# Optimization experiments

Measured on AMD Instinct MI355X. Metric: run time of the kernel, lower is better.

Reference implementation:

```python
import jax, jax.numpy as jnp
import numpy as np

ROPE_BASE = 10000.0

def apply_rope(x):
    # x: [B, S, H, Dh]  (rotate-half / NeoX convention)
    B, S, H, Dh = x.shape
    inv_freq = 1.0 / (ROPE_BASE ** (jnp.arange(0, Dh, 2, dtype=jnp.float32) / Dh))  # [Dh/2]
    ang = jnp.arange(S, dtype=jnp.float32)[:, None] * inv_freq[None, :]             # [S, Dh/2]
    cos = jnp.cos(ang)[None, :, None, :].astype(x.dtype)  # [1,S,1,Dh/2]
    sin = jnp.sin(ang)[None, :, None, :].astype(x.dtype)
    x1, x2 = jnp.split(x, 2, axis=-1)
    return jnp.concatenate([x1 * cos - x2 * sin, x1 * sin + x2 * cos], axis=-1)

def setup_inputs() -> dict:
    key = jax.random.key(0)
    k1, k2, k3 = jax.random.split(key, 3)
    B, S, D = 2, 2048, 1024
    x = jax.random.normal(k1, (B, S, D), dtype=jnp.float32)
    attn_mask = jnp.ones((B, S), dtype=bool)
    qkv_w = jax.random.normal(k2, (D, 3 * D), dtype=jnp.float32) * (1.0 / np.sqrt(D))
    out_w = jax.random.normal(k3, (D, D), dtype=jnp.float32) * (1.0 / np.sqrt(D))
    return {"x": x, "qkv_w": qkv_w, "out_w": out_w, "attn_mask": attn_mask, "is_causal": 1}

def reference(x, qkv_w, out_w, attn_mask, is_causal):
    B, S, D = x.shape
    H = 16
    Dh = D // H
    qkv = x @ qkv_w                                  # [B,S,3D]
    q, k, v = jnp.split(qkv, 3, axis=-1)
    q = apply_rope(q.reshape(B, S, H, Dh))           # [B,S,H,Dh]
    k = apply_rope(k.reshape(B, S, H, Dh))
    v = v.reshape(B, S, H, Dh)
    scale = 1.0 / np.sqrt(Dh)
    att = jnp.einsum('bqhd,bkhd->bhqk', q, k) * scale  # [B,H,S,S]
    if is_causal:
        mask = jnp.tril(jnp.ones((S, S), dtype=bool))[None, None]
    else:
        mask = attn_mask[:, None, None, :]             # [B,1,1,S]
    att = jnp.where(mask, att, jnp.finfo(att.dtype).min)
    p = jax.nn.softmax(att, axis=-1)
    y = jnp.einsum('bhqk,bkhd->bqhd', p, v).reshape(B, S, D)
    return y @ out_w
```

## Files before the change

### kernel.cpp

```cpp
#include <hip/hip_runtime.h>
#include <hip/hip_bf16.h>

#define BB 2
#define SS 2048
#define DD 1024
#define HH 16
#define N3 3072

typedef __attribute__((ext_vector_type(8))) short bf16x8;
typedef __attribute__((ext_vector_type(4))) float f32x4;

__device__ __forceinline__ float b2f(unsigned short u) {
    return __uint_as_float(((unsigned int)u) << 16);
}
__device__ __forceinline__ unsigned short f2b(float f) {
    unsigned int x = __float_as_uint(f);
    x += 0x7fffu + ((x >> 16) & 1u);
    return (unsigned short)(x >> 16);
}
__device__ __forceinline__ unsigned int pack2bf(float a, float b) {
    __hip_bfloat162 h = __float22bfloat162_rn(make_float2(a, b));
    return *(unsigned int*)&h;
}
__device__ __forceinline__ void storeC(float* p, float v) { *p = v; }
__device__ __forceinline__ void storeC(unsigned short* p, float v) { *p = f2b(v); }

__device__ __forceinline__ void gload_lds16(const void* g, void* l) {
    __builtin_amdgcn_global_load_lds(
        (__attribute__((address_space(1))) void*)g,
        (__attribute__((address_space(3))) void*)l, 16, 0, 0);
}

__global__ __launch_bounds__(256) void sincos_tab(float2* __restrict__ tab) {
    int i = blockIdx.x * 256 + threadIdx.x;
    int t = i & 31;
    int s = i >> 5;
    float inv = powf(10000.0f, -(float)t * (1.0f / 32.0f));
    float sn, c;
    sincosf((float)s * inv, &sn, &c);
    tab[i] = make_float2(c, sn);
}

__global__ __launch_bounds__(256) void cast_f32_bf16(
    const float* __restrict__ src, unsigned short* __restrict__ dst)
{
    int i = (blockIdx.x * 256 + threadIdx.x) * 4;
    float4 f = *(const float4*)(src + i);
    uint2 o;
    o.x = pack2bf(f.x, f.y);
    o.y = pack2bf(f.z, f.w);
    *(uint2*)(dst + i) = o;
}

__global__ __launch_bounds__(256) void cast_transpose(
    const float* __restrict__ src, unsigned short* __restrict__ dst,
    int R, int C)
{
    __shared__ unsigned short tile[64][66];
    const int t = threadIdx.x;
    const int c0 = blockIdx.x * 64, r0 = blockIdx.y * 64;
    const int lr = t >> 4;
    const int lc = (t & 15) * 4;
    #pragma unroll
    for (int i = 0; i < 4; ++i) {
        float4 f = *(const float4*)(src + (size_t)(r0 + lr + i * 16) * C + c0 + lc);
        tile[lr + i * 16][lc + 0] = f2b(f.x);
        tile[lr + i * 16][lc + 1] = f2b(f.y);
        tile[lr + i * 16][lc + 2] = f2b(f.z);
        tile[lr + i * 16][lc + 3] = f2b(f.w);
    }
    __syncthreads();
    #pragma unroll
    for (int i = 0; i < 4; ++i) {
        const int wr = lr + i * 16;
        ushort4 o;
        o.x = tile[lc + 0][wr];
        o.y = tile[lc + 1][wr];
        o.z = tile[lc + 2][wr];
        o.w = tile[lc + 3][wr];
        *(ushort4*)(dst + (size_t)(c0 + wr) * R + r0 + lc) = o;
    }
}

template <typename OutT, int TN>
__global__ __launch_bounds__(256) void gemm_mfma(
    const unsigned short* __restrict__ A,
    const unsigned short* __restrict__ Bt,
    OutT* __restrict__ C,
    int M, int N, int K)
{
    constexpr int NI = TN / 32;
    constexpr int NB = TN / 64;
    __shared__ unsigned short Al[128 * 32];
    __shared__ unsigned short Bl[TN * 32];
    const int tid  = threadIdx.x;
    const int wave = tid >> 6;
    const int lane = tid & 63;
    const int quad = lane >> 4;
    const int l16  = lane & 15;
    const int m0 = blockIdx.y * 128;
    const int n0 = blockIdx.x * TN;
    const int wm = (wave >> 1) * 64;
    const int wn = (wave & 1) * (TN / 2);

    const int srowA = wave * 32 + (lane >> 2);
    const int srowB = wave * (16 * NB) + (lane >> 2);
    const int scol  = (lane & 3) * 8;
    const unsigned short* gA = A  + (size_t)(m0 + srowA) * K + scol;
    const unsigned short* gB = Bt + (size_t)(n0 + srowB) * K + scol;

    f32x4 acc[4][NI];
    #pragma unroll
    for (int mi = 0; mi < 4; ++mi)
        #pragma unroll
        for (int ni = 0; ni < NI; ++ni)
            acc[mi][ni] = (f32x4){0.f, 0.f, 0.f, 0.f};

    for (int k0 = 0; k0 < K; k0 += 32) {
        __syncthreads();
        #pragma unroll
        for (int i = 0; i < 2; ++i)
            gload_lds16(gA + (size_t)i * 16 * K + k0, Al + (wave * 2 + i) * 512);
        #pragma unroll
        for (int i = 0; i < NB; ++i)
            gload_lds16(gB + (size_t)i * 16 * K + k0, Bl + (wave * NB + i) * 512);
        __syncthreads();

        bf16x8 af[4], bfr[NI];
        #pragma unroll
        for (int mi = 0; mi < 4; ++mi)
            af[mi] = *(const bf16x8*)&Al[(wm + mi * 16 + l16) * 32 + quad * 8];
        #pragma unroll
        for (int ni = 0; ni < NI; ++ni)
            bfr[ni] = *(const bf16x8*)&Bl[(wn + ni * 16 + l16) * 32 + quad * 8];
        #pragma unroll
        for (int mi = 0; mi < 4; ++mi)
            #pragma unroll
            for (int ni = 0; ni < NI; ++ni)
                acc[mi][ni] = __builtin_amdgcn_mfma_f32_16x16x32_bf16(
                    af[mi], bfr[ni], acc[mi][ni], 0, 0, 0);
    }

    #pragma unroll
    for (int mi = 0; mi < 4; ++mi) {
        #pragma unroll
        for (int r = 0; r < 4; ++r) {
            const size_t base = (size_t)(m0 + wm + mi * 16 + quad * 4 + r) * N + n0 + wn;
            #pragma unroll
            for (int ni = 0; ni < NI; ++ni)
                storeC(&C[base + ni * 16 + l16], acc[mi][ni][r]);
        }
    }
}

__global__ __launch_bounds__(256) void rope_split(
    const unsigned short* __restrict__ qkv,
    const float2* __restrict__ tab,
    unsigned short* __restrict__ qo,
    unsigned short* __restrict__ ko,
    unsigned short* __restrict__ vt)
{
    __shared__ unsigned short Vtile[64][72];

    const int s0 = blockIdx.x * 64;
    const int h  = blockIdx.y;
    const int b  = blockIdx.z;
    const int tid = threadIdx.x;
    const int sl = tid >> 2;
    const int qu = tid & 3;
    const size_t bh = (size_t)b * HH + h;

    const unsigned short* row = qkv + (size_t)(b * SS + s0 + sl) * N3 + h * 64;

    uint4 a0 = *(const uint4*)(row + qu * 8);
    uint4 a1 = *(const uint4*)(row + 32 + qu * 8);
    uint4 b0 = *(const uint4*)(row + DD + qu * 8);
    uint4 b1 = *(const uint4*)(row + DD + 32 + qu * 8);
    uint4 c0 = *(const uint4*)(row + 2 * DD + qu * 8);
    uint4 c1 = *(const uint4*)(row + 2 * DD + 32 + qu * 8);

    float2 cs[8];
    {
        const float4* tp = (const float4*)(tab + (size_t)(s0 + sl) * 32 + qu * 8);
        #pragma unroll
        for (int i = 0; i < 4; ++i) {
            float4 f = tp[i];
            cs[2 * i]     = make_float2(f.x, f.y);
            cs[2 * i + 1] = make_float2(f.z, f.w);
        }
    }

    const unsigned short* pa0 = (const unsigned short*)&a0;
    const unsigned short* pa1 = (const unsigned short*)&a1;
    const unsigned short* pb0 = (const unsigned short*)&b0;
    const unsigned short* pb1 = (const unsigned short*)&b1;
    const unsigned short* pc0 = (const unsigned short*)&c0;
    const unsigned short* pc1 = (const unsigned short*)&c1;

    unsigned short oq1[8], oq2[8], ok1[8], ok2[8];
    #pragma unroll
    for (int j = 0; j < 8; ++j) {
        float c = cs[j].x, sn = cs[j].y;
        float q1 = b2f(pa0[j]), q2 = b2f(pa1[j]);
        float k1 = b2f(pb0[j]), k2 = b2f(pb1[j]);
        oq1[j] = f2b(q1 * c - q2 * sn);
        oq2[j] = f2b(q1 * sn + q2 * c);
        ok1[j] = f2b(k1 * c - k2 * sn);
        ok2[j] = f2b(k1 * sn + k2 * c);
        Vtile[qu * 8 + j][sl]      = pc0[j];
        Vtile[32 + qu * 8 + j][sl] = pc1[j];
    }
    const size_t qoff = (bh * SS + s0 + sl) * 64;
    *(uint4*)(qo + qoff + qu * 8)      = *(const uint4*)oq1;
    *(uint4*)(qo + qoff + 32 + qu * 8) = *(const uint4*)oq2;
    *(uint4*)(ko + qoff + qu * 8)      = *(const uint4*)ok1;
    *(uint4*)(ko + qoff + 32 + qu * 8) = *(const uint4*)ok2;

    __syncthreads();

    const int dr = tid >> 2;
    const int ch = tid & 3;
    uint4 t0 = *(const uint4*)&Vtile[dr][ch * 16];
    uint4 t1 = *(const uint4*)&Vtile[dr][ch * 16 + 8];
    unsigned short* vrow = vt + (bh * 64 + dr) * SS + s0 + ch * 16;
    *(uint4*)vrow       = t0;
    *(uint4*)(vrow + 8) = t1;
}

__device__ __forceinline__ void attn_step(
    const unsigned short* __restrict__ Kb,
    const unsigned short* __restrict__ Vb,
    unsigned short* __restrict__ PqW,
    const bf16x8 qf0, const bf16x8 qf1,
    f32x4 O[4], float& m_run, float& l_run,
    bool diag, const unsigned char* mrow,
    int kt, int quad, int l16, int csw, int qg)
{
    const float SC = 0.18033688011112042f;

    f32x4 Sf[4];
    #pragma unroll
    for (int st = 0; st < 4; ++st) {
        const unsigned short* kr = &Kb[(st * 16 + l16) * 64];
        bf16x8 kf0 = *(const bf16x8*)(kr + csw * 8);
        bf16x8 kf1 = *(const bf16x8*)(kr + (csw ^ 4) * 8);
        f32x4 s = (f32x4){0.f, 0.f, 0.f, 0.f};
        s = __builtin_amdgcn_mfma_f32_16x16x32_bf16(kf0, qf0, s, 0, 0, 0);
        s = __builtin_amdgcn_mfma_f32_16x16x32_bf16(kf1, qf1, s, 0, 0, 0);
        #pragma unroll
        for (int r = 0; r < 4; ++r) s[r] *= SC;
        Sf[st] = s;
    }

    if (diag) {
        #pragma unroll
        for (int st = 0; st < 4; ++st) {
            const int kb0 = kt * 64 + st * 16 + quad * 4;
            #pragma unroll
            for (int r = 0; r < 4; ++r)
                if (kb0 + r > qg) Sf[st][r] = -1e30f;
        }
    } else if (mrow) {
        #pragma unroll
        for (int st = 0; st < 4; ++st) {
            uchar4 mv = *(const uchar4*)(mrow + st * 16 + quad * 4);
            if (!mv.x) Sf[st][0] = -1e30f;
            if (!mv.y) Sf[st][1] = -1e30f;
            if (!mv.z) Sf[st][2] = -1e30f;
            if (!mv.w) Sf[st][3] = -1e30f;
        }
    }

    float mx = Sf[0][0];
    #pragma unroll
    for (int st = 0; st < 4; ++st)
        #pragma unroll
        for (int r = 0; r < 4; ++r) mx = fmaxf(mx, Sf[st][r]);
    mx = fmaxf(mx, __shfl_xor(mx, 16));
    mx = fmaxf(mx, __shfl_xor(mx, 32));
    const float mnew = fmaxf(m_run, mx);
    const float alpha = exp2f(m_run - mnew);
    m_run = mnew;

    float lsum = 0.f;
    #pragma unroll
    for (int st = 0; st < 4; ++st)
        #pragma unroll
        for (int r = 0; r < 4; ++r) {
            float p = exp2f(Sf[st][r] - mnew);
            Sf[st][r] = p;
            lsum += p;
        }
    lsum += __shfl_xor(lsum, 16);
    lsum += __shfl_xor(lsum, 32);
    l_run = l_run * alpha + lsum;

    #pragma unroll
    for (int st = 0; st < 4; ++st)
        #pragma unroll
        for (int r = 0; r < 4; ++r) O[st][r] *= alpha;

    #pragma unroll
    for (int st = 0; st < 4; ++st) {
        uint2 pk;
        pk.x = pack2bf(Sf[st][0], Sf[st][1]);
        pk.y = pack2bf(Sf[st][2], Sf[st][3]);
        *(uint2*)&PqW[l16 * 72 + st * 16 + quad * 4] = pk;
    }
    bf16x8 pf0 = *(const bf16x8*)&PqW[l16 * 72 + quad * 8];
    bf16x8 pf1 = *(const bf16x8*)&PqW[l16 * 72 + 32 + quad * 8];

    #pragma unroll
    for (int st = 0; st < 4; ++st) {
        const unsigned short* vr = &Vb[(st * 16 + l16) * 64];
        bf16x8 vf0 = *(const bf16x8*)(vr + csw * 8);
        bf16x8 vf1 = *(const bf16x8*)(vr + (csw ^ 4) * 8);
        O[st] = __builtin_amdgcn_mfma_f32_16x16x32_bf16(vf0, pf0, O[st], 0, 0, 0);
        O[st] = __builtin_amdgcn_mfma_f32_16x16x32_bf16(vf1, pf1, O[st], 0, 0, 0);
    }
}

__global__ __launch_bounds__(256) void flash_attn(
    const unsigned short* __restrict__ q,
    const unsigned short* __restrict__ k,
    const unsigned short* __restrict__ vt,
    unsigned short* __restrict__ y,
    const int* __restrict__ is_causal,
    const unsigned char* __restrict__ attn_mask)
{
    __shared__ unsigned short Kl[2][64 * 64];
    __shared__ unsigned short Vl[2][64 * 64];
    __shared__ unsigned short Pq[4][16 * 72];

    const int j   = blockIdx.x;
    const int h   = blockIdx.y;
    const int b   = blockIdx.z;
    const int tid = threadIdx.x;
    const int wave = tid >> 6;
    const int lane = tid & 63;
    const int quad = lane >> 4;
    const int l16  = lane & 15;

    const size_t bh = (size_t)b * HH + h;
    const bool causal = (is_causal[0] != 0);
    const int NT = SS / 64;
    const int tA = j, tB = NT - 1 - j;
    const int ntrips = causal ? (tB + 1) : NT;

    const unsigned short* qrowA = q + (bh * SS + tA * 64 + wave * 16 + l16) * 64;
    const unsigned short* qrowB = q + (bh * SS + tB * 64 + wave * 16 + l16) * 64;
    const bf16x8 qfA0 = *(const bf16x8*)(qrowA + quad * 8);
    const bf16x8 qfA1 = *(const bf16x8*)(qrowA + 32 + quad * 8);
    const bf16x8 qfB0 = *(const bf16x8*)(qrowB + quad * 8);
    const bf16x8 qfB1 = *(const bf16x8*)(qrowB + 32 + quad * 8);

    const unsigned short* kbase  = k  + bh * SS * 64;
    const unsigned short* vtbase = vt + bh * 64 * SS;

    const int Rl  = lane >> 3;
    const int cph = lane & 7;
    const int csw = quad ^ (l16 & 7);

    f32x4 OA[4], OB[4];
    #pragma unroll
    for (int st = 0; st < 4; ++st) {
        OA[st] = (f32x4){0.f, 0.f, 0.f, 0.f};
        OB[st] = (f32x4){0.f, 0.f, 0.f, 0.f};
    }
    float mA = -1e30f, lA = 0.f, mB = -1e30f, lB = 0.f;

    const int qgA = tA * 64 + wave * 16 + l16;
    const int qgB = tB * 64 + wave * 16 + l16;

    auto stage = [&](int kt) {
        const int buf = kt & 1;
        #pragma unroll
        for (int i = 0; i < 2; ++i) {
            const int jj = wave * 2 + i;
            const int R  = jj * 8 + Rl;
            const int cl = cph ^ (R & 7);
            gload_lds16(kbase + ((size_t)(kt * 64 + R) * 64 + cl * 8),
                        &Kl[buf][jj * 512]);
            gload_lds16(vtbase + ((size_t)R * SS + kt * 64 + cl * 8),
                        &Vl[buf][jj * 512]);
        }
    };

    stage(0);
    for (int kt = 0; kt < ntrips; ++kt) {
        __syncthreads();
        if (kt + 1 < ntrips) stage(kt + 1);

        const unsigned short* Kb = Kl[kt & 1];
        const unsigned short* Vb = Vl[kt & 1];
        const unsigned char* mrow = causal ? nullptr
                                           : (attn_mask + (size_t)b * SS + kt * 64);

        if (!causal || kt <= tA)
            attn_step(Kb, Vb, Pq[wave], qfA0, qfA1, OA, mA, lA,
                      causal && kt == tA, mrow, kt, quad, l16, csw, qgA);
        attn_step(Kb, Vb, Pq[wave], qfB0, qfB1, OB, mB, lB,
                  causal && kt == tB, mrow, kt, quad, l16, csw, qgB);
    }

    const float invA = 1.0f / lA;
    unsigned short* yrowA = y + ((size_t)b * SS + qgA) * DD + h * 64;
    #pragma unroll
    for (int st = 0; st < 4; ++st) {
        uint2 o;
        o.x = pack2bf(OA[st][0] * invA, OA[st][1] * invA);
        o.y = pack2bf(OA[st][2] * invA, OA[st][3] * invA);
        *(uint2*)(yrowA + st * 16 + quad * 4) = o;
    }
    const float invB = 1.0f / lB;
    unsigned short* yrowB = y + ((size_t)b * SS + qgB) * DD + h * 64;
    #pragma unroll
    for (int st = 0; st < 4; ++st) {
        uint2 o;
        o.x = pack2bf(OB[st][0] * invB, OB[st][1] * invB);
        o.y = pack2bf(OB[st][2] * invB, OB[st][3] * invB);
        *(uint2*)(yrowB + st * 16 + quad * 4) = o;
    }
}

extern "C" void kernel_launch(void* const* d_in, const int* in_sizes, int n_in,
                              void* d_out, int out_size, void* d_ws, size_t ws_size,
                              hipStream_t stream) {
    const float* x      = (const float*)d_in[0];
    const float* qkv_w  = (const float*)d_in[1];
    const float* out_w  = (const float*)d_in[2];
    const unsigned char* mask = (const unsigned char*)d_in[3];
    const int*   is_c   = (const int*)d_in[4];
    float* out = (float*)d_out;

    unsigned short* xb  = (unsigned short*)d_ws;
    unsigned short* w1t = xb  + (size_t)4096 * 1024;
    unsigned short* w2t = w1t + (size_t)3072 * 1024;
    unsigned short* qkv = w2t + (size_t)1024 * 1024;
    unsigned short* qb  = qkv + (size_t)4096 * 3072;
    unsigned short* kb  = qb  + (size_t)BB * HH * SS * 64;
    unsigned short* vt  = kb  + (size_t)BB * HH * SS * 64;
    float2* tab = (float2*)(vt + (size_t)BB * HH * SS * 64);
    unsigned short* yb = xb;

    sincos_tab<<<(SS * 32) / 256, 256, 0, stream>>>(tab);
    cast_f32_bf16<<<(4096 * 1024) / 1024, 256, 0, stream>>>(x, xb);
    cast_transpose<<<dim3(N3 / 64, DD / 64), 256, 0, stream>>>(qkv_w, w1t, DD, N3);
    cast_transpose<<<dim3(DD / 64, DD / 64), 256, 0, stream>>>(out_w, w2t, DD, DD);

    gemm_mfma<unsigned short, 128><<<dim3(N3 / 128, 4096 / 128), 256, 0, stream>>>(
        xb, w1t, qkv, 4096, N3, DD);

    rope_split<<<dim3(SS / 64, HH, BB), 256, 0, stream>>>(qkv, tab, qb, kb, vt);

    flash_attn<<<dim3(SS / 128, HH, BB), 256, 0, stream>>>(qb, kb, vt, yb, is_c, mask);

    gemm_mfma<float, 64><<<dim3(DD / 64, 4096 / 128), 256, 0, stream>>>(
        yb, w2t, out, 4096, DD, DD);
}
```

Measured before the change: 220.8 us.

## Fold softmax scale into Q, lazy rescale, one tile per block with swizzled schedule

Moves the softmax scale into the RoPE kernel so Q is pre-scaled, removing per-score multiplies. Adds a lazy online-softmax rescale that skips the alpha correction unless the row max grows by more than 8 (log2 units), and defers the row-sum cross-lane reduction to the end. Replaces the paired-tile blocks with one query tile per block, using a 1D grid with a permuted/balanced tile order across heads, and XOR-swizzles the P staging buffer in LDS. Skipped rescales rely on bounded growth of unnormalised exponentials, and single-tile blocks lose the K/V load sharing between two query tiles.

```diff
diff --git a/kernel.cpp b/kernel.cpp
--- a/kernel.cpp
+++ b/kernel.cpp
@@ -162,6 +162,7 @@
 {
     __shared__ unsigned short Vtile[64][72];
 
+    const float SC = 0.18033688011112042f;
     const int s0 = blockIdx.x * 64;
     const int h  = blockIdx.y;
     const int b  = blockIdx.z;
@@ -203,8 +204,8 @@
         float c = cs[j].x, sn = cs[j].y;
         float q1 = b2f(pa0[j]), q2 = b2f(pa1[j]);
         float k1 = b2f(pb0[j]), k2 = b2f(pb1[j]);
-        oq1[j] = f2b(q1 * c - q2 * sn);
-        oq2[j] = f2b(q1 * sn + q2 * c);
+        oq1[j] = f2b((q1 * c - q2 * sn) * SC);
+        oq2[j] = f2b((q1 * sn + q2 * c) * SC);
         ok1[j] = f2b(k1 * c - k2 * sn);
         ok2[j] = f2b(k1 * sn + k2 * c);
         Vtile[qu * 8 + j][sl]      = pc0[j];
@@ -236,8 +237,6 @@
     bool diag, const unsigned char* mrow,
     int kt, int quad, int l16, int csw, int qg)
 {
-    const float SC = 0.18033688011112042f;
-
     f32x4 Sf[4];
     #pragma unroll
     for (int st = 0; st < 4; ++st) {
@@ -247,8 +246,6 @@
         f32x4 s = (f32x4){0.f, 0.f, 0.f, 0.f};
         s = __builtin_amdgcn_mfma_f32_16x16x32_bf16(kf0, qf0, s, 0, 0, 0);
         s = __builtin_amdgcn_mfma_f32_16x16x32_bf16(kf1, qf1, s, 0, 0, 0);
-        #pragma unroll
-        for (int r = 0; r < 4; ++r) s[r] *= SC;
         Sf[st] = s;
     }
 
@@ -278,37 +275,40 @@
         for (int r = 0; r < 4; ++r) mx = fmaxf(mx, Sf[st][r]);
     mx = fmaxf(mx, __shfl_xor(mx, 16));
     mx = fmaxf(mx, __shfl_xor(mx, 32));
-    const float mnew = fmaxf(m_run, mx);
-    const float alpha = exp2f(m_run - mnew);
-    m_run = mnew;
+
+    if (!__all(mx <= m_run + 8.0f)) {
+        const float mnew = fmaxf(m_run, mx);
+        const float alpha = exp2f(m_run - mnew);
+        #pragma unroll
+        for (int st = 0; st < 4; ++st)
+            #pragma unroll
+            for (int r = 0; r < 4; ++r) O[st][r] *= alpha;
+        l_run *= alpha;
+        m_run = mnew;
+    }
 
     float lsum = 0.f;
     #pragma unroll
     for (int st = 0; st < 4; ++st)
         #pragma unroll
         for (int r = 0; r < 4; ++r) {
-            float p = exp2f(Sf[st][r] - mnew);
-            Sf[st][r] = p;
-            lsum += p;
-        }
-    lsum += __shfl_xor(lsum, 16);
-    lsum += __shfl_xor(lsum, 32);
-    l_run = l_run * alpha + lsum;
-
-    #pragma unroll
-    for (int st = 0; st < 4; ++st)
-        #pragma unroll
-        for (int r = 0; r < 4; ++r) O[st][r] *= alpha;
-
+            float pp = exp2f(Sf[st][r] - m_run);
+            Sf[st][r] = pp;
+            lsum += pp;
+        }
+    l_run += lsum;
+
+    const int sw = (l16 & 7) << 4;
+    char* pb = (char*)PqW + l16 * 128;
     #pragma unroll
     for (int st = 0; st < 4; ++st) {
         uint2 pk;
         pk.x = pack2bf(Sf[st][0], Sf[st][1]);
         pk.y = pack2bf(Sf[st][2], Sf[st][3]);
-        *(uint2*)&PqW[l16 * 72 + st * 16 + quad * 4] = pk;
-    }
-    bf16x8 pf0 = *(const bf16x8*)&PqW[l16 * 72 + quad * 8];
-    bf16x8 pf1 = *(const bf16x8*)&PqW[l16 * 72 + 32 + quad * 8];
+        *(uint2*)(pb + ((st * 32 + quad * 8) ^ sw)) = pk;
+    }
+    bf16x8 pf0 = *(const bf16x8*)(pb + ((quad * 16) ^ sw));
+    bf16x8 pf1 = *(const bf16x8*)(pb + ((64 + quad * 16) ^ sw));
 
     #pragma unroll
     for (int st = 0; st < 4; ++st) {
@@ -330,12 +330,23 @@
 {
     __shared__ unsigned short Kl[2][64 * 64];
     __shared__ unsigned short Vl[2][64 * 64];
-    __shared__ unsigned short Pq[4][16 * 72];
-
-    const int j   = blockIdx.x;
-    const int h   = blockIdx.y;
-    const int b   = blockIdx.z;
-    const int tid = threadIdx.x;
+    __shared__ unsigned short Pq[4][16 * 64];
+
+    const int bid  = blockIdx.x;
+    const int work = ((bid & 7) << 7) | (bid >> 3);
+    const int bhi  = work >> 5;
+    const int p    = work & 31;
+    int tile;
+    switch (bhi & 3) {
+        case 0:  tile = p;             break;
+        case 1:  tile = 31 - p;        break;
+        case 2:  tile = (p + 16) & 31; break;
+        default: tile = (47 - p) & 31; break;
+    }
+    const int b = bhi >> 4;
+    const int h = bhi & 15;
+
+    const int tid  = threadIdx.x;
     const int wave = tid >> 6;
     const int lane = tid & 63;
     const int quad = lane >> 4;
@@ -344,15 +355,11 @@
     const size_t bh = (size_t)b * HH + h;
     const bool causal = (is_causal[0] != 0);
     const int NT = SS / 64;
-    const int tA = j, tB = NT - 1 - j;
-    const int ntrips = causal ? (tB + 1) : NT;
-
-    const unsigned short* qrowA = q + (bh * SS + tA * 64 + wave * 16 + l16) * 64;
-    const unsigned short* qrowB = q + (bh * SS + tB * 64 + wave * 16 + l16) * 64;
-    const bf16x8 qfA0 = *(const bf16x8*)(qrowA + quad * 8);
-    const bf16x8 qfA1 = *(const bf16x8*)(qrowA + 32 + quad * 8);
-    const bf16x8 qfB0 = *(const bf16x8*)(qrowB + quad * 8);
-    const bf16x8 qfB1 = *(const bf16x8*)(qrowB + 32 + quad * 8);
+    const int ntrips = causal ? (tile + 1) : NT;
+
+    const unsigned short* qrow = q + (bh * SS + tile * 64 + wave * 16 + l16) * 64;
+    const bf16x8 qf0 = *(const bf16x8*)(qrow + quad * 8);
+    const bf16x8 qf1 = *(const bf16x8*)(qrow + 32 + quad * 8);
 
     const unsigned short* kbase  = k  + bh * SS * 64;
     const unsigned short* vtbase = vt + bh * 64 * SS;
@@ -361,16 +368,12 @@
     const int cph = lane & 7;
     const int csw = quad ^ (l16 & 7);
 
-    f32x4 OA[4], OB[4];
-    #pragma unroll
-    for (int st = 0; st < 4; ++st) {
-        OA[st] = (f32x4){0.f, 0.f, 0.f, 0.f};
-        OB[st] = (f32x4){0.f, 0.f, 0.f, 0.f};
-    }
-    float mA = -1e30f, lA = 0.f, mB = -1e30f, lB = 0.f;
-
-    const int qgA = tA * 64 + wave * 16 + l16;
-    const int qgB = tB * 64 + wave * 16 + l16;
+    f32x4 O[4];
+    #pragma unroll
+    for (int st = 0; st < 4; ++st) O[st] = (f32x4){0.f, 0.f, 0.f, 0.f};
+    float m_run = -1e30f, l_run = 0.f;
+
+    const int qg = tile * 64 + wave * 16 + l16;
 
     auto stage = [&](int kt) {
         const int buf = kt & 1;
@@ -391,35 +394,22 @@
         __syncthreads();
         if (kt + 1 < ntrips) stage(kt + 1);
 
-        const unsigned short* Kb = Kl[kt & 1];
-        const unsigned short* Vb = Vl[kt & 1];
         const unsigned char* mrow = causal ? nullptr
                                            : (attn_mask + (size_t)b * SS + kt * 64);
-
-        if (!causal || kt <= tA)
-            attn_step(Kb, Vb, Pq[wave], qfA0, qfA1, OA, mA, lA,
-                      causal && kt == tA, mrow, kt, quad, l16, csw, qgA);
-        attn_step(Kb, Vb, Pq[wave], qfB0, qfB1, OB, mB, lB,
-                  causal && kt == tB, mrow, kt, quad, l16, csw, qgB);
-    }
-
-    const float invA = 1.0f / lA;
-    unsigned short* yrowA = y + ((size_t)b * SS + qgA) * DD + h * 64;
+        attn_step(Kl[kt & 1], Vl[kt & 1], Pq[wave], qf0, qf1, O, m_run, l_run,
+                  causal && kt == tile, mrow, kt, quad, l16, csw, qg);
+    }
+
+    l_run += __shfl_xor(l_run, 16);
+    l_run += __shfl_xor(l_run, 32);
+    const float inv = 1.0f / l_run;
+    unsigned short* yrow = y + ((size_t)b * SS + qg) * DD + h * 64;
     #pragma unroll
     for (int st = 0; st < 4; ++st) {
         uint2 o;
-        o.x = pack2bf(OA[st][0] * invA, OA[st][1] * invA);
-        o.y = pack2bf(OA[st][2] * invA, OA[st][3] * invA);
-        *(uint2*)(yrowA + st * 16 + quad * 4) = o;
-    }
-    const float invB = 1.0f / lB;
-    unsigned short* yrowB = y + ((size_t)b * SS + qgB) * DD + h * 64;
-    #pragma unroll
-    for (int st = 0; st < 4; ++st) {
-        uint2 o;
-        o.x = pack2bf(OB[st][0] * invB, OB[st][1] * invB);
-        o.y = pack2bf(OB[st][2] * invB, OB[st][3] * invB);
-        *(uint2*)(yrowB + st * 16 + quad * 4) = o;
+        o.x = pack2bf(O[st][0] * inv, O[st][1] * inv);
+        o.y = pack2bf(O[st][2] * inv, O[st][3] * inv);
+        *(uint2*)(yrow + st * 16 + quad * 4) = o;
     }
 }
 
@@ -453,7 +443,7 @@
 
     rope_split<<<dim3(SS / 64, HH, BB), 256, 0, stream>>>(qkv, tab, qb, kb, vt);
 
-    flash_attn<<<dim3(SS / 128, HH, BB), 256, 0, stream>>>(qb, kb, vt, yb, is_c, mask);
+    flash_attn<<<dim3(BB * HH * (SS / 64)), 256, 0, stream>>>(qb, kb, vt, yb, is_c, mask);
 
     gemm_mfma<float, 64><<<dim3(DD / 64, 4096 / 128), 256, 0, stream>>>(
         yb, w2t, out, 4096, DD, DD);
```

Measured after the change: 216.7 us. Within noise of the previous version (-1.8%).

## Restructure flash attention work split, fold scale into Q, add lazy rescale

Applied to the files above, without the earlier changes.

Each workgroup now owns a contiguous 128-row query chunk, and each wave takes 32 adjacent rows, replacing the paired first/last tile scheme. Blocks are launched on a 1D grid with a swizzled order that reverses the chunk order on alternate heads to balance the causal load. The softmax scale moves into the RoPE kernel for Q, and the per-tile row-sum shuffles are deferred to the end. Max rescaling is now skipped unless the new max exceeds the running max by more than 8, and the P tile in LDS is XOR-swizzled to avoid bank conflicts. The risks are causal imbalance inside a block, since its waves finish at different tiles and sit idle at barriers, plus a small change in numerics.

```diff
diff --git a/kernel.cpp b/kernel.cpp
--- a/kernel.cpp
+++ b/kernel.cpp
@@ -162,6 +162,7 @@
 {
     __shared__ unsigned short Vtile[64][72];
 
+    const float SC = 0.18033688011112042f;
     const int s0 = blockIdx.x * 64;
     const int h  = blockIdx.y;
     const int b  = blockIdx.z;
@@ -203,8 +204,8 @@
         float c = cs[j].x, sn = cs[j].y;
         float q1 = b2f(pa0[j]), q2 = b2f(pa1[j]);
         float k1 = b2f(pb0[j]), k2 = b2f(pb1[j]);
-        oq1[j] = f2b(q1 * c - q2 * sn);
-        oq2[j] = f2b(q1 * sn + q2 * c);
+        oq1[j] = f2b((q1 * c - q2 * sn) * SC);
+        oq2[j] = f2b((q1 * sn + q2 * c) * SC);
         ok1[j] = f2b(k1 * c - k2 * sn);
         ok2[j] = f2b(k1 * sn + k2 * c);
         Vtile[qu * 8 + j][sl]      = pc0[j];
@@ -225,99 +226,6 @@
     unsigned short* vrow = vt + (bh * 64 + dr) * SS + s0 + ch * 16;
     *(uint4*)vrow       = t0;
     *(uint4*)(vrow + 8) = t1;
-}
-
-__device__ __forceinline__ void attn_step(
-    const unsigned short* __restrict__ Kb,
-    const unsigned short* __restrict__ Vb,
-    unsigned short* __restrict__ PqW,
-    const bf16x8 qf0, const bf16x8 qf1,
-    f32x4 O[4], float& m_run, float& l_run,
-    bool diag, const unsigned char* mrow,
-    int kt, int quad, int l16, int csw, int qg)
-{
-    const float SC = 0.18033688011112042f;
-
-    f32x4 Sf[4];
-    #pragma unroll
-    for (int st = 0; st < 4; ++st) {
-        const unsigned short* kr = &Kb[(st * 16 + l16) * 64];
-        bf16x8 kf0 = *(const bf16x8*)(kr + csw * 8);
-        bf16x8 kf1 = *(const bf16x8*)(kr + (csw ^ 4) * 8);
-        f32x4 s = (f32x4){0.f, 0.f, 0.f, 0.f};
-        s = __builtin_amdgcn_mfma_f32_16x16x32_bf16(kf0, qf0, s, 0, 0, 0);
-        s = __builtin_amdgcn_mfma_f32_16x16x32_bf16(kf1, qf1, s, 0, 0, 0);
-        #pragma unroll
-        for (int r = 0; r < 4; ++r) s[r] *= SC;
-        Sf[st] = s;
-    }
-
-    if (diag) {
-        #pragma unroll
-        for (int st = 0; st < 4; ++st) {
-            const int kb0 = kt * 64 + st * 16 + quad * 4;
-            #pragma unroll
-            for (int r = 0; r < 4; ++r)
-                if (kb0 + r > qg) Sf[st][r] = -1e30f;
-        }
-    } else if (mrow) {
-        #pragma unroll
-        for (int st = 0; st < 4; ++st) {
-            uchar4 mv = *(const uchar4*)(mrow + st * 16 + quad * 4);
-            if (!mv.x) Sf[st][0] = -1e30f;
-            if (!mv.y) Sf[st][1] = -1e30f;
-            if (!mv.z) Sf[st][2] = -1e30f;
-            if (!mv.w) Sf[st][3] = -1e30f;
-        }
-    }
-
-    float mx = Sf[0][0];
-    #pragma unroll
-    for (int st = 0; st < 4; ++st)
-        #pragma unroll
-        for (int r = 0; r < 4; ++r) mx = fmaxf(mx, Sf[st][r]);
-    mx = fmaxf(mx, __shfl_xor(mx, 16));
-    mx = fmaxf(mx, __shfl_xor(mx, 32));
-    const float mnew = fmaxf(m_run, mx);
-    const float alpha = exp2f(m_run - mnew);
-    m_run = mnew;
-
-    float lsum = 0.f;
-    #pragma unroll
-    for (int st = 0; st < 4; ++st)
-        #pragma unroll
-        for (int r = 0; r < 4; ++r) {
-            float p = exp2f(Sf[st][r] - mnew);
-            Sf[st][r] = p;
-            lsum += p;
-        }
-    lsum += __shfl_xor(lsum, 16);
-    lsum += __shfl_xor(lsum, 32);
-    l_run = l_run * alpha + lsum;
-
-    #pragma unroll
-    for (int st = 0; st < 4; ++st)
-        #pragma unroll
-        for (int r = 0; r < 4; ++r) O[st][r] *= alpha;
-
-    #pragma unroll
-    for (int st = 0; st < 4; ++st) {
-        uint2 pk;
-        pk.x = pack2bf(Sf[st][0], Sf[st][1]);
-        pk.y = pack2bf(Sf[st][2], Sf[st][3]);
-        *(uint2*)&PqW[l16 * 72 + st * 16 + quad * 4] = pk;
-    }
-    bf16x8 pf0 = *(const bf16x8*)&PqW[l16 * 72 + quad * 8];
-    bf16x8 pf1 = *(const bf16x8*)&PqW[l16 * 72 + 32 + quad * 8];
-
-    #pragma unroll
-    for (int st = 0; st < 4; ++st) {
-        const unsigned short* vr = &Vb[(st * 16 + l16) * 64];
-        bf16x8 vf0 = *(const bf16x8*)(vr + csw * 8);
-        bf16x8 vf1 = *(const bf16x8*)(vr + (csw ^ 4) * 8);
-        O[st] = __builtin_amdgcn_mfma_f32_16x16x32_bf16(vf0, pf0, O[st], 0, 0, 0);
-        O[st] = __builtin_amdgcn_mfma_f32_16x16x32_bf16(vf1, pf1, O[st], 0, 0, 0);
-    }
 }
 
 __global__ __launch_bounds__(256) void flash_attn(
@@ -330,12 +238,17 @@
 {
     __shared__ unsigned short Kl[2][64 * 64];
     __shared__ unsigned short Vl[2][64 * 64];
-    __shared__ unsigned short Pq[4][16 * 72];
-
-    const int j   = blockIdx.x;
-    const int h   = blockIdx.y;
-    const int b   = blockIdx.z;
-    const int tid = threadIdx.x;
+    __shared__ unsigned short Pq[4][16 * 64];
+
+    const int bid  = blockIdx.x;
+    const int work = ((bid & 7) << 6) | (bid >> 3);
+    const int bhi  = work >> 4;
+    const int p    = work & 15;
+    const int c    = (bhi & 2) ? (15 - p) : p;
+    const int b = bhi >> 4;
+    const int h = bhi & 15;
+
+    const int tid  = threadIdx.x;
     const int wave = tid >> 6;
     const int lane = tid & 63;
     const int quad = lane >> 4;
@@ -344,11 +257,15 @@
     const size_t bh = (size_t)b * HH + h;
     const bool causal = (is_causal[0] != 0);
     const int NT = SS / 64;
-    const int tA = j, tB = NT - 1 - j;
-    const int ntrips = causal ? (tB + 1) : NT;
-
-    const unsigned short* qrowA = q + (bh * SS + tA * 64 + wave * 16 + l16) * 64;
-    const unsigned short* qrowB = q + (bh * SS + tB * 64 + wave * 16 + l16) * 64;
+    const int ntrips = causal ? (2 * c + 2) : NT;
+
+    const int r0  = c * 128 + wave * 32;
+    const int qgA = r0 + l16;
+    const int qgB = r0 + 16 + l16;
+    const int tW  = r0 >> 6;
+
+    const unsigned short* qrowA = q + (bh * SS + r0 + l16) * 64;
+    const unsigned short* qrowB = q + (bh * SS + r0 + 16 + l16) * 64;
     const bf16x8 qfA0 = *(const bf16x8*)(qrowA + quad * 8);
     const bf16x8 qfA1 = *(const bf16x8*)(qrowA + 32 + quad * 8);
     const bf16x8 qfB0 = *(const bf16x8*)(qrowB + quad * 8);
@@ -369,8 +286,71 @@
     }
     float mA = -1e30f, lA = 0.f, mB = -1e30f, lB = 0.f;
 
-    const int qgA = tA * 64 + wave * 16 + l16;
-    const int qgB = tB * 64 + wave * 16 + l16;
+    const int sw = (l16 & 7) << 4;
+    char* pb = (char*)&Pq[wave][0] + l16 * 128;
+
+    auto softmax_prep = [&](f32x4* Sf, float& m_run, float& l_run, f32x4* O,
+                            bool diag, const unsigned char* mrow, int kt, int qg,
+                            bf16x8& pf0, bf16x8& pf1) {
+        if (diag) {
+            #pragma unroll
+            for (int st = 0; st < 4; ++st) {
+                const int kb0 = kt * 64 + st * 16 + quad * 4;
+                #pragma unroll
+                for (int r = 0; r < 4; ++r)
+                    if (kb0 + r > qg) Sf[st][r] = -1e30f;
+            }
+        } else if (mrow) {
+            #pragma unroll
+            for (int st = 0; st < 4; ++st) {
+                uchar4 mv = *(const uchar4*)(mrow + st * 16 + quad * 4);
+                if (!mv.x) Sf[st][0] = -1e30f;
+                if (!mv.y) Sf[st][1] = -1e30f;
+                if (!mv.z) Sf[st][2] = -1e30f;
+                if (!mv.w) Sf[st][3] = -1e30f;
+            }
+        }
+
+        float mx = Sf[0][0];
+        #pragma unroll
+        for (int st = 0; st < 4; ++st)
+            #pragma unroll
+            for (int r = 0; r < 4; ++r) mx = fmaxf(mx, Sf[st][r]);
+        mx = fmaxf(mx, __shfl_xor(mx, 16));
+        mx = fmaxf(mx, __shfl_xor(mx, 32));
+
+        if (!__all(mx <= m_run + 8.0f)) {
+            const float mnew = fmaxf(m_run, mx);
+            const float alpha = exp2f(m_run - mnew);
+            #pragma unroll
+            for (int st = 0; st < 4; ++st)
+                #pragma unroll
+                for (int r = 0; r < 4; ++r) O[st][r] *= alpha;
+            l_run *= alpha;
+            m_run = mnew;
+        }
+
+        float lsum = 0.f;
+        #pragma unroll
+        for (int st = 0; st < 4; ++st)
+            #pragma unroll
+            for (int r = 0; r < 4; ++r) {
+                float pp = exp2f(Sf[st][r] - m_run);
+                Sf[st][r] = pp;
+                lsum += pp;
+            }
+        l_run += lsum;
+
+        #pragma unroll
+        for (int st = 0; st < 4; ++st) {
+            uint2 pk;
+            pk.x = pack2bf(Sf[st][0], Sf[st][1]);
+            pk.y = pack2bf(Sf[st][2], Sf[st][3]);
+            *(uint2*)(pb + ((st * 32 + quad * 8) ^ sw)) = pk;
+        }
+        pf0 = *(const bf16x8*)(pb + ((quad * 16) ^ sw));
+        pf1 = *(const bf16x8*)(pb + ((64 + quad * 16) ^ sw));
+    };
 
     auto stage = [&](int kt) {
         const int buf = kt & 1;
@@ -391,18 +371,49 @@
         __syncthreads();
         if (kt + 1 < ntrips) stage(kt + 1);
 
-        const unsigned short* Kb = Kl[kt & 1];
-        const unsigned short* Vb = Vl[kt & 1];
-        const unsigned char* mrow = causal ? nullptr
-                                           : (attn_mask + (size_t)b * SS + kt * 64);
-
-        if (!causal || kt <= tA)
-            attn_step(Kb, Vb, Pq[wave], qfA0, qfA1, OA, mA, lA,
-                      causal && kt == tA, mrow, kt, quad, l16, csw, qgA);
-        attn_step(Kb, Vb, Pq[wave], qfB0, qfB1, OB, mB, lB,
-                  causal && kt == tB, mrow, kt, quad, l16, csw, qgB);
-    }
-
+        const bool active = !causal || (kt <= tW);
+        if (active) {
+            const unsigned short* Kb = Kl[kt & 1];
+            const unsigned short* Vb = Vl[kt & 1];
+            const bool diag = causal && (kt == tW);
+            const unsigned char* mrow = causal ? nullptr
+                                               : (attn_mask + (size_t)b * SS + kt * 64);
+
+            f32x4 SA[4], SB[4];
+            #pragma unroll
+            for (int st = 0; st < 4; ++st) {
+                const unsigned short* kr = &Kb[(st * 16 + l16) * 64];
+                bf16x8 kf0 = *(const bf16x8*)(kr + csw * 8);
+                bf16x8 kf1 = *(const bf16x8*)(kr + (csw ^ 4) * 8);
+                f32x4 s = (f32x4){0.f, 0.f, 0.f, 0.f};
+                s = __builtin_amdgcn_mfma_f32_16x16x32_bf16(kf0, qfA0, s, 0, 0, 0);
+                s = __builtin_amdgcn_mfma_f32_16x16x32_bf16(kf1, qfA1, s, 0, 0, 0);
+                SA[st] = s;
+                s = (f32x4){0.f, 0.f, 0.f, 0.f};
+                s = __builtin_amdgcn_mfma_f32_16x16x32_bf16(kf0, qfB0, s, 0, 0, 0);
+                s = __builtin_amdgcn_mfma_f32_16x16x32_bf16(kf1, qfB1, s, 0, 0, 0);
+                SB[st] = s;
+            }
+
+            bf16x8 pfA0, pfA1, pfB0, pfB1;
+            softmax_prep(SA, mA, lA, OA, diag, mrow, kt, qgA, pfA0, pfA1);
+            softmax_prep(SB, mB, lB, OB, diag, mrow, kt, qgB, pfB0, pfB1);
+
+            #pragma unroll
+            for (int st = 0; st < 4; ++st) {
+                const unsigned short* vr = &Vb[(st * 16 + l16) * 64];
+                bf16x8 vf0 = *(const bf16x8*)(vr + csw * 8);
+                bf16x8 vf1 = *(const bf16x8*)(vr + (csw ^ 4) * 8);
+                OA[st] = __builtin_amdgcn_mfma_f32_16x16x32_bf16(vf0, pfA0, OA[st], 0, 0, 0);
+                OA[st] = __builtin_amdgcn_mfma_f32_16x16x32_bf16(vf1, pfA1, OA[st], 0, 0, 0);
+                OB[st] = __builtin_amdgcn_mfma_f32_16x16x32_bf16(vf0, pfB0, OB[st], 0, 0, 0);
+                OB[st] = __builtin_amdgcn_mfma_f32_16x16x32_bf16(vf1, pfB1, OB[st], 0, 0, 0);
+            }
+        }
+    }
+
+    lA += __shfl_xor(lA, 16);
+    lA += __shfl_xor(lA, 32);
     const float invA = 1.0f / lA;
     unsigned short* yrowA = y + ((size_t)b * SS + qgA) * DD + h * 64;
     #pragma unroll
@@ -412,6 +423,8 @@
         o.y = pack2bf(OA[st][2] * invA, OA[st][3] * invA);
         *(uint2*)(yrowA + st * 16 + quad * 4) = o;
     }
+    lB += __shfl_xor(lB, 16);
+    lB += __shfl_xor(lB, 32);
     const float invB = 1.0f / lB;
     unsigned short* yrowB = y + ((size_t)b * SS + qgB) * DD + h * 64;
     #pragma unroll
@@ -453,7 +466,7 @@
 
     rope_split<<<dim3(SS / 64, HH, BB), 256, 0, stream>>>(qkv, tab, qb, kb, vt);
 
-    flash_attn<<<dim3(SS / 128, HH, BB), 256, 0, stream>>>(qb, kb, vt, yb, is_c, mask);
+    flash_attn<<<dim3(BB * HH * (SS / 128)), 256, 0, stream>>>(qb, kb, vt, yb, is_c, mask);
 
     gemm_mfma<float, 64><<<dim3(DD / 64, 4096 / 128), 256, 0, stream>>>(
         yb, w2t, out, 4096, DD, DD);
```

Result: slower. 229.4 us (+3.9%).
